# Kernel tuning notes

Measured on AMD Instinct MI355X. Metric: run time of the kernel, lower is better.

The kernel has to match this reference:

```python
import jax, jax.numpy as jnp
import numpy as np
from jax import lax

B, N, K = 8, 4096, 16          # clouds, points per cloud, knn neighbors
RATIO = 0.5
M = int(N * RATIO)             # sampled points per cloud (fps ratio)
C_IN, C_OUT = 64, 128
EPS = 1e-5                      # BatchNorm eps


def setup_inputs() -> dict:
    key = jax.random.key(0)
    ks = jax.random.split(key, 4)
    x = jax.random.normal(ks[0], (B * N, C_IN), jnp.float32)
    pos = jax.random.uniform(ks[1], (B * N, 3), jnp.float32)
    batch = jnp.repeat(jnp.arange(B, dtype=jnp.int32), N)
    W = jax.random.normal(ks[2], (C_IN, C_OUT), jnp.float32) / np.sqrt(C_IN).astype(np.float32)
    b = jnp.zeros((C_OUT,), jnp.float32)
    gamma = jnp.ones((C_OUT,), jnp.float32)
    beta = jnp.zeros((C_OUT,), jnp.float32)
    return {"x": x, "pos": pos, "batch": batch, "W": W, "b": b, "gamma": gamma, "beta": beta}


def _fps(pos_c):
    # Farthest point sampling on one cloud. pos_c: [N,3] -> [M] local indices.
    # Deterministic start at index 0 (reference for torch_cluster.fps).
    def step(carry, _):
        dmin, last = carry
        d = jnp.sum((pos_c - pos_c[last]) ** 2, axis=-1)   # [N]
        dmin = jnp.minimum(dmin, d)
        nxt = jnp.argmax(dmin).astype(jnp.int32)
        return (dmin, nxt), last
    init = (jnp.full((pos_c.shape[0],), jnp.inf, pos_c.dtype), jnp.int32(0))
    _, idx = lax.scan(step, init, None, length=M)
    return idx


def _knn(pos_c, qpos_c):
    # k nearest original points for each sampled point. [N,3],[M,3] -> [M,K].
    d = jnp.sum((qpos_c[:, None, :] - pos_c[None, :, :]) ** 2, axis=-1)  # [M,N]
    _, idx = lax.top_k(-d, K)
    return idx


def reference(x, pos, batch, W, b, gamma, beta):
    pos_b = pos.reshape(B, N, 3)
    fps_idx = jax.vmap(_fps)(pos_b)                                       # [B,M]
    new_pos_b = jnp.take_along_axis(pos_b, fps_idx[:, :, None], axis=1)   # [B,M,3]
    nbr = jax.vmap(_knn)(pos_b, new_pos_b)                                # [B,M,K]

    # mlp: Linear -> BatchNorm1d (training-mode batch stats) -> GELU
    h = x @ W + b                                                         # [B*N,C_OUT]
    mu = jnp.mean(h, axis=0)
    var = jnp.mean((h - mu) ** 2, axis=0)
    h = (h - mu) * lax.rsqrt(var + EPS) * gamma + beta
    h = jax.nn.gelu(h, approximate=False)
    h_b = h.reshape(B, N, C_OUT)

    # gather neighbor features; scatter-max over edge_index[0] == max over K
    # (each sampled point has exactly K incoming edges)
    feats = jax.vmap(lambda hb, nb: hb[nb])(h_b, nbr)                     # [B,M,K,C_OUT]
    new_x = jnp.max(feats, axis=2).reshape(B * M, C_OUT)
    new_pos = new_pos_b.reshape(B * M, 3)
    new_batch = jnp.repeat(jnp.arange(B, dtype=batch.dtype), M)
    return (new_x, new_pos, new_batch)
```

## Files before the change

### kernel.cpp

```cpp
#include <hip/hip_runtime.h>
#include <math.h>

#define NB 8
#define NN 4096
#define MM 2048
#define KNN_K 16
#define CIN 64
#define COUT 128
#define BN_EPS 1e-5f

typedef float v2f __attribute__((ext_vector_type(2)));

__device__ __forceinline__ v2f pk_add(v2f a, v2f b) {
  v2f r;
  asm("v_pk_add_f32 %0, %1, %2" : "=v"(r) : "v"(a), "v"(b));
  return r;
}
__device__ __forceinline__ v2f pk_mul(v2f a, v2f b) {
  v2f r;
  asm("v_pk_mul_f32 %0, %1, %2" : "=v"(r) : "v"(a), "v"(b));
  return r;
}

__device__ __forceinline__ double pack_key(float d, unsigned code) {
  return __longlong_as_double(
      (long long)(((unsigned long long)__float_as_uint(d) << 32) | code));
}
__device__ __forceinline__ unsigned unpack_code(double v) {
  return (unsigned)((unsigned long long)__double_as_longlong(v) &
                    0xFFFFFFFFull);
}

__device__ __forceinline__ float sqdist_np(float dx, float dy, float dz) {
  return __fadd_rn(__fadd_rn(__fmul_rn(dx, dx), __fmul_rn(dy, dy)),
                   __fmul_rn(dz, dz));
}

#define DPP_MAX_LEVEL(best, ctrl, rmask)                                     \
  {                                                                          \
    const int _lo = __builtin_amdgcn_update_dpp(                             \
        __double2loint(best), __double2loint(best), (ctrl), (rmask), 0xf,    \
        false);                                                              \
    const int _hi = __builtin_amdgcn_update_dpp(                             \
        __double2hiint(best), __double2hiint(best), (ctrl), (rmask), 0xf,    \
        false);                                                              \
    best = fmax(best, __hiloint2double(_hi, _lo));                           \
  }
#define DPP_MIN_LEVEL(best, ctrl, rmask)                                     \
  {                                                                          \
    const int _lo = __builtin_amdgcn_update_dpp(                             \
        __double2loint(best), __double2loint(best), (ctrl), (rmask), 0xf,    \
        false);                                                              \
    const int _hi = __builtin_amdgcn_update_dpp(                             \
        __double2hiint(best), __double2hiint(best), (ctrl), (rmask), 0xf,    \
        false);                                                              \
    best = fmin(best, __hiloint2double(_hi, _lo));                           \
  }

__global__ __launch_bounds__(256) void k_fps_gemm(
    const float* __restrict__ pos, const float* __restrict__ x,
    const float* __restrict__ W, const float* __restrict__ bias,
    float* __restrict__ h, float* __restrict__ gsum,
    float* __restrict__ gsumsq, int* __restrict__ fps_idx,
    float* __restrict__ out_pos, float* __restrict__ out_batch) {
  __shared__ __align__(16) char smem_raw[57472];
  const int tid = threadIdx.x;

  if (blockIdx.x < NB) {
    float* xs = (float*)smem_raw;
    float* ys = xs + NN;
    float* zs = ys + NN;
    int* idxs = (int*)(smem_raw + 49152);
    double* red = (double*)(smem_raw + 57344);
    const int b = blockIdx.x;
    const float* posc = pos + (size_t)b * NN * 3;
    for (int i = tid; i < NN; i += 256) {
      xs[i] = posc[i * 3 + 0];
      ys[i] = posc[i * 3 + 1];
      zs[i] = posc[i * 3 + 2];
    }
    __syncthreads();

    v2f pxv[8], pyv[8], pzv[8];
    double key[16];
    const unsigned code_base = (unsigned)(NN - 1 - tid * 16);
#pragma unroll
    for (int u = 0; u < 8; ++u) {
      const int p = tid * 16 + 2 * u;
      pxv[u] = (v2f){xs[p], xs[p + 1]};
      pyv[u] = (v2f){ys[p], ys[p + 1]};
      pzv[u] = (v2f){zs[p], zs[p + 1]};
    }
#pragma unroll
    for (int s = 0; s < 16; ++s)
      key[s] = __hiloint2double(0x7f800000, (int)(code_base - s));

    const int lane = tid & 63, wv = tid >> 6;
    int last = 0;
    if (tid == 0) idxs[0] = 0;
    float lx = xs[0], ly = ys[0], lz = zs[0];
    for (int m = 1; m < MM; ++m) {
      const v2f nlx = {-lx, -lx}, nly = {-ly, -ly}, nlz = {-lz, -lz};
      double b0 = 0.0, b1 = 0.0, b2 = 0.0, b3 = 0.0;
#pragma unroll
      for (int u = 0; u < 8; ++u) {
        const v2f dx = pk_add(pxv[u], nlx);
        const v2f dy = pk_add(pyv[u], nly);
        const v2f dz = pk_add(pzv[u], nlz);
        const v2f d2 =
            pk_add(pk_add(pk_mul(dx, dx), pk_mul(dy, dy)), pk_mul(dz, dz));
        const int s0 = 2 * u, s1 = 2 * u + 1;
        const float n0 =
            fminf(__int_as_float(__double2hiint(key[s0])), d2.x);
        const float n1 =
            fminf(__int_as_float(__double2hiint(key[s1])), d2.y);
        key[s0] = __hiloint2double(__float_as_int(n0), (int)(code_base - s0));
        key[s1] = __hiloint2double(__float_as_int(n1), (int)(code_base - s1));
        switch (u & 3) {
          case 0: b0 = fmax(b0, fmax(key[s0], key[s1])); break;
          case 1: b1 = fmax(b1, fmax(key[s0], key[s1])); break;
          case 2: b2 = fmax(b2, fmax(key[s0], key[s1])); break;
          default: b3 = fmax(b3, fmax(key[s0], key[s1])); break;
        }
      }
      double best = fmax(fmax(b0, b1), fmax(b2, b3));
      DPP_MAX_LEVEL(best, 0x121, 0xf);
      DPP_MAX_LEVEL(best, 0x122, 0xf);
      DPP_MAX_LEVEL(best, 0x124, 0xf);
      DPP_MAX_LEVEL(best, 0x128, 0xf);
      DPP_MAX_LEVEL(best, 0x142, 0xa);
      DPP_MAX_LEVEL(best, 0x143, 0xc);
      const int par = (m & 1) * 4;
      if (lane == 63) red[par + wv] = best;
      __syncthreads();
      const double f = fmax(fmax(red[par + 0], red[par + 1]),
                            fmax(red[par + 2], red[par + 3]));
      last = (NN - 1) - (int)unpack_code(f);
      if (tid == 0) idxs[m] = last;
      lx = xs[last];
      ly = ys[last];
      lz = zs[last];
    }
    __syncthreads();
    for (int m = tid; m < MM; m += 256) {
      const int p = idxs[m];
      const int o = b * MM + m;
      fps_idx[o] = p;
      out_pos[o * 3 + 0] = xs[p];
      out_pos[o * 3 + 1] = ys[p];
      out_pos[o * 3 + 2] = zs[p];
      out_batch[o] = (float)b;
    }
  } else {
    float* Wl = (float*)smem_raw;
    float* xl = Wl + CIN * COUT;
    float* bsum = (float*)(smem_raw + 49152);
    float* bsq = bsum + COUT;
    const int bid = blockIdx.x - NB;
    const int r0 = bid * 64;
    for (int i = tid; i < CIN * COUT; i += 256) Wl[i] = W[i];
    for (int i = tid; i < 64 * CIN; i += 256) xl[i] = x[(size_t)r0 * CIN + i];
    if (tid < 2 * COUT) bsum[tid] = 0.f;
    __syncthreads();
    const int cg = tid & 31, rg = tid >> 5;
    const int c = cg * 4;
    float acc[8][4];
#pragma unroll
    for (int j = 0; j < 8; ++j)
#pragma unroll
      for (int t = 0; t < 4; ++t) acc[j][t] = 0.f;
    for (int k = 0; k < CIN; ++k) {
      const float4 wk = *(const float4*)&Wl[k * COUT + c];
#pragma unroll
      for (int j = 0; j < 8; ++j) {
        const float xv = xl[(rg * 8 + j) * CIN + k];
        acc[j][0] = fmaf(xv, wk.x, acc[j][0]);
        acc[j][1] = fmaf(xv, wk.y, acc[j][1]);
        acc[j][2] = fmaf(xv, wk.z, acc[j][2]);
        acc[j][3] = fmaf(xv, wk.w, acc[j][3]);
      }
    }
    const float4 bb = *(const float4*)&bias[c];
    float s0 = 0, s1 = 0, s2 = 0, s3 = 0, q0 = 0, q1 = 0, q2 = 0, q3 = 0;
#pragma unroll
    for (int j = 0; j < 8; ++j) {
      float4 hv;
      hv.x = acc[j][0] + bb.x;
      hv.y = acc[j][1] + bb.y;
      hv.z = acc[j][2] + bb.z;
      hv.w = acc[j][3] + bb.w;
      *(float4*)&h[(size_t)(r0 + rg * 8 + j) * COUT + c] = hv;
      s0 += hv.x; s1 += hv.y; s2 += hv.z; s3 += hv.w;
      q0 += hv.x * hv.x; q1 += hv.y * hv.y;
      q2 += hv.z * hv.z; q3 += hv.w * hv.w;
    }
    atomicAdd(&bsum[c + 0], s0); atomicAdd(&bsum[c + 1], s1);
    atomicAdd(&bsum[c + 2], s2); atomicAdd(&bsum[c + 3], s3);
    atomicAdd(&bsq[c + 0], q0);  atomicAdd(&bsq[c + 1], q1);
    atomicAdd(&bsq[c + 2], q2);  atomicAdd(&bsq[c + 3], q3);
    __syncthreads();
    if (tid < COUT) {
      atomicAdd(&gsum[tid], bsum[tid]);
      atomicAdd(&gsumsq[tid], bsq[tid]);
    }
  }
}

__device__ __forceinline__ float gelu_exact(float v) {
  return 0.5f * v * (1.0f + erff(v * 0.70710678118654752f));
}

__global__ __launch_bounds__(256) void k_knn(
    const float* __restrict__ pos, const int* __restrict__ fps_idx,
    const float* __restrict__ h, const float* __restrict__ gsum,
    const float* __restrict__ gsumsq, const float* __restrict__ gamma,
    const float* __restrict__ beta, float* __restrict__ out_x) {
  __shared__ float dc[4][NN];
  __shared__ float sc[COUT], sh[COUT];
  const int tid = threadIdx.x, lane = tid & 63, wv = tid >> 6;
  if (tid < COUT) {
    const float n = (float)(NB * NN);
    const float mu = gsum[tid] / n;
    const float var = gsumsq[tid] / n - mu * mu;
    const float rs = rsqrtf(var + BN_EPS);
    const float s = rs * gamma[tid];
    sc[tid] = s;
    sh[tid] = beta[tid] - mu * s;
  }
  __syncthreads();
  const int b = blockIdx.x & 7;
  const int m = (blockIdx.x >> 3) * 4 + wv;
  const int q = b * MM + m;
  const int qi = fps_idx[q];
  const float* posc = pos + (size_t)b * NN * 3;
  const float qx = posc[qi * 3 + 0], qy = posc[qi * 3 + 1],
              qz = posc[qi * 3 + 2];
  float* dcw = dc[wv];
  const double DINF = __longlong_as_double(0x7FF0000000000000LL);
  double gmin[8];
#pragma unroll
  for (int g = 0; g < 8; ++g) gmin[g] = DINF;
#pragma unroll
  for (int s = 0; s < 64; ++s) {
    const int p = s * 64 + lane;
    const float d = sqdist_np(posc[p * 3 + 0] - qx, posc[p * 3 + 1] - qy,
                              posc[p * 3 + 2] - qz);
    dcw[p] = d;
    gmin[s >> 3] = fmin(gmin[s >> 3], pack_key(d, (unsigned)p));
  }
  double lmin = gmin[0];
#pragma unroll
  for (int g = 1; g < 8; ++g) lmin = fmin(lmin, gmin[g]);

  int nbr[KNN_K];
#pragma unroll
  for (int r = 0; r < KNN_K; ++r) {
    double v = lmin;
    DPP_MIN_LEVEL(v, 0x121, 0xf);
    DPP_MIN_LEVEL(v, 0x122, 0xf);
    DPP_MIN_LEVEL(v, 0x124, 0xf);
    DPP_MIN_LEVEL(v, 0x128, 0xf);
    DPP_MIN_LEVEL(v, 0x142, 0xa);
    DPP_MIN_LEVEL(v, 0x143, 0xc);
    const unsigned p =
        (unsigned)__builtin_amdgcn_readlane(__double2loint(v), 63);
    nbr[r] = (int)p;
    if (lane == (int)(p & 63)) {
      dcw[p] = __int_as_float(0x7f800000);
      const int g = (int)(p >> 9);
      double nm = DINF;
      const int base = g * 8 * 64 + lane;
#pragma unroll
      for (int j = 0; j < 8; ++j) {
        const int pp = base + j * 64;
        nm = fmin(nm, pack_key(dcw[pp], (unsigned)pp));
      }
#pragma unroll
      for (int gg = 0; gg < 8; ++gg)
        if (gg == g) gmin[gg] = nm;
      lmin = gmin[0];
#pragma unroll
      for (int gg = 1; gg < 8; ++gg) lmin = fmin(lmin, gmin[gg]);
    }
  }

  const float* hb = h + (size_t)b * NN * COUT;
  const float PINF = __int_as_float(0x7f800000);
  float mx0 = -PINF, mn0 = PINF, mx1 = -PINF, mn1 = PINF;
#pragma unroll
  for (int r = 0; r < KNN_K; ++r) {
    const float* row = hb + (size_t)nbr[r] * COUT;
    const float a = row[lane], c = row[lane + 64];
    mx0 = fmaxf(mx0, a);
    mn0 = fminf(mn0, a);
    mx1 = fmaxf(mx1, c);
    mn1 = fminf(mn1, c);
  }
  const float sc0 = sc[lane], sh0 = sh[lane];
  const float sc1 = sc[lane + 64], sh1 = sh[lane + 64];
  const float o0 = fmaxf(gelu_exact(fmaf(mx0, sc0, sh0)),
                         gelu_exact(fmaf(mn0, sc0, sh0)));
  const float o1 = fmaxf(gelu_exact(fmaf(mx1, sc1, sh1)),
                         gelu_exact(fmaf(mn1, sc1, sh1)));
  out_x[(size_t)q * COUT + lane] = o0;
  out_x[(size_t)q * COUT + lane + 64] = o1;
}

extern "C" void kernel_launch(void* const* d_in, const int* in_sizes, int n_in,
                              void* d_out, int out_size, void* d_ws,
                              size_t ws_size, hipStream_t stream) {
  const float* x = (const float*)d_in[0];
  const float* pos = (const float*)d_in[1];
  const float* W = (const float*)d_in[3];
  const float* bias = (const float*)d_in[4];
  const float* gamma = (const float*)d_in[5];
  const float* beta = (const float*)d_in[6];

  float* out_x = (float*)d_out;
  float* out_pos = out_x + (size_t)NB * MM * COUT;
  float* out_batch = out_pos + (size_t)NB * MM * 3;

  char* ws = (char*)d_ws;
  float* h = (float*)ws;
  float* gsum = (float*)(ws + (size_t)16777216);
  float* gsumsq = gsum + COUT;
  int* fps_idx = (int*)(gsumsq + COUT);

  (void)hipMemsetAsync(gsum, 0, 2 * COUT * sizeof(float), stream);
  hipLaunchKernelGGL(k_fps_gemm, dim3(NB + 512), dim3(256), 0, stream, pos, x,
                     W, bias, h, gsum, gsumsq, fps_idx, out_pos, out_batch);
  hipLaunchKernelGGL(k_knn, dim3(4096), dim3(256), 0, stream, pos, fps_idx, h,
                     gsum, gsumsq, gamma, beta, out_x);
}
```

Measured before the change: 1.236 ms.

## Fuse FPS, GEMM and kNN into one persistent kernel streaming FPS indices

Merges the two kernels into one persistent launch. The 8 FPS blocks publish each sampled index to a global flag array as soon as it is chosen. 504 worker blocks first compute the GEMM tiles with BN statistics, wait on a global counter, then run kNN and the gather-max on published queries while FPS is still running. The kNN step now recomputes distances instead of caching them in LDS, which frees shared memory for higher occupancy. The design depends on all blocks being co-resident (spin-waits) and adds polling traffic and global atomics.

```diff
diff --git a/kernel.cpp b/kernel.cpp
--- a/kernel.cpp
+++ b/kernel.cpp
@@ -8,6 +8,8 @@
 #define CIN 64
 #define COUT 128
 #define BN_EPS 1e-5f
+#define NWORK 504
+#define NTILES 512
 
 typedef float v2f __attribute__((ext_vector_type(2)));
 
@@ -57,21 +59,27 @@
     best = fmin(best, __hiloint2double(_hi, _lo));                           \
   }
 
-__global__ __launch_bounds__(256) void k_fps_gemm(
+__device__ __forceinline__ float gelu_exact(float v) {
+  return 0.5f * v * (1.0f + erff(v * 0.70710678118654752f));
+}
+
+__global__ __launch_bounds__(256, 3) void k_fused(
     const float* __restrict__ pos, const float* __restrict__ x,
     const float* __restrict__ W, const float* __restrict__ bias,
+    const float* __restrict__ gamma, const float* __restrict__ beta,
     float* __restrict__ h, float* __restrict__ gsum,
-    float* __restrict__ gsumsq, int* __restrict__ fps_idx,
+    float* __restrict__ gsumsq, int* __restrict__ pub,
+    int* __restrict__ gemm_done, float* __restrict__ out_x,
     float* __restrict__ out_pos, float* __restrict__ out_batch) {
-  __shared__ __align__(16) char smem_raw[57472];
+  __shared__ __align__(16) char smem_raw[50176];
   const int tid = threadIdx.x;
+  const int lane = tid & 63, wv = tid >> 6;
 
   if (blockIdx.x < NB) {
     float* xs = (float*)smem_raw;
     float* ys = xs + NN;
     float* zs = ys + NN;
-    int* idxs = (int*)(smem_raw + 49152);
-    double* red = (double*)(smem_raw + 57344);
+    double* red = (double*)(smem_raw + 49152);
     const int b = blockIdx.x;
     const float* posc = pos + (size_t)b * NN * 3;
     for (int i = tid; i < NN; i += 256) {
@@ -95,10 +103,15 @@
     for (int s = 0; s < 16; ++s)
       key[s] = __hiloint2double(0x7f800000, (int)(code_base - s));
 
-    const int lane = tid & 63, wv = tid >> 6;
     int last = 0;
-    if (tid == 0) idxs[0] = 0;
     float lx = xs[0], ly = ys[0], lz = zs[0];
+    if (tid == 0) {
+      __hip_atomic_store(&pub[b * MM], 1, __ATOMIC_RELAXED,
+                         __HIP_MEMORY_SCOPE_AGENT);
+      out_pos[(size_t)(b * MM) * 3 + 0] = lx;
+      out_pos[(size_t)(b * MM) * 3 + 1] = ly;
+      out_pos[(size_t)(b * MM) * 3 + 2] = lz;
+    }
     for (int m = 1; m < MM; ++m) {
       const v2f nlx = {-lx, -lx}, nly = {-ly, -ly}, nlz = {-lz, -lz};
       double b0 = 0.0, b1 = 0.0, b2 = 0.0, b3 = 0.0;
@@ -136,174 +149,201 @@
       const double f = fmax(fmax(red[par + 0], red[par + 1]),
                             fmax(red[par + 2], red[par + 3]));
       last = (NN - 1) - (int)unpack_code(f);
-      if (tid == 0) idxs[m] = last;
       lx = xs[last];
       ly = ys[last];
       lz = zs[last];
-    }
-    __syncthreads();
-    for (int m = tid; m < MM; m += 256) {
-      const int p = idxs[m];
-      const int o = b * MM + m;
-      fps_idx[o] = p;
-      out_pos[o * 3 + 0] = xs[p];
-      out_pos[o * 3 + 1] = ys[p];
-      out_pos[o * 3 + 2] = zs[p];
-      out_batch[o] = (float)b;
-    }
+      if (tid == 0) {
+        const int o = b * MM + m;
+        __hip_atomic_store(&pub[o], last + 1, __ATOMIC_RELAXED,
+                           __HIP_MEMORY_SCOPE_AGENT);
+        out_pos[(size_t)o * 3 + 0] = lx;
+        out_pos[(size_t)o * 3 + 1] = ly;
+        out_pos[(size_t)o * 3 + 2] = lz;
+      }
+    }
+    for (int m = tid; m < MM; m += 256) out_batch[b * MM + m] = (float)b;
   } else {
+    const int wkr = blockIdx.x - NB;
     float* Wl = (float*)smem_raw;
     float* xl = Wl + CIN * COUT;
     float* bsum = (float*)(smem_raw + 49152);
     float* bsq = bsum + COUT;
-    const int bid = blockIdx.x - NB;
-    const int r0 = bid * 64;
-    for (int i = tid; i < CIN * COUT; i += 256) Wl[i] = W[i];
-    for (int i = tid; i < 64 * CIN; i += 256) xl[i] = x[(size_t)r0 * CIN + i];
-    if (tid < 2 * COUT) bsum[tid] = 0.f;
+#pragma unroll 1
+    for (int rep = 0; rep < 2; ++rep) {
+      if (rep == 1 && wkr >= NTILES - NWORK) break;
+      const int t = rep ? (NWORK + wkr) : wkr;
+      const int r0 = t * 64;
+      for (int i = tid; i < CIN * COUT; i += 256) Wl[i] = W[i];
+      for (int i = tid; i < 64 * CIN; i += 256)
+        xl[i] = x[(size_t)r0 * CIN + i];
+      bsum[tid] = 0.f;
+      __syncthreads();
+      const int cg = tid & 31, rg = tid >> 5;
+      const int c = cg * 4;
+      float acc[8][4];
+#pragma unroll
+      for (int j = 0; j < 8; ++j)
+#pragma unroll
+        for (int tt = 0; tt < 4; ++tt) acc[j][tt] = 0.f;
+      for (int k = 0; k < CIN; ++k) {
+        const float4 wk = *(const float4*)&Wl[k * COUT + c];
+#pragma unroll
+        for (int j = 0; j < 8; ++j) {
+          const float xv = xl[(rg * 8 + j) * CIN + k];
+          acc[j][0] = fmaf(xv, wk.x, acc[j][0]);
+          acc[j][1] = fmaf(xv, wk.y, acc[j][1]);
+          acc[j][2] = fmaf(xv, wk.z, acc[j][2]);
+          acc[j][3] = fmaf(xv, wk.w, acc[j][3]);
+        }
+      }
+      const float4 bb = *(const float4*)&bias[c];
+      float s0 = 0, s1 = 0, s2 = 0, s3 = 0, q0 = 0, q1 = 0, q2 = 0, q3 = 0;
+#pragma unroll
+      for (int j = 0; j < 8; ++j) {
+        float4 hv;
+        hv.x = acc[j][0] + bb.x;
+        hv.y = acc[j][1] + bb.y;
+        hv.z = acc[j][2] + bb.z;
+        hv.w = acc[j][3] + bb.w;
+        *(float4*)&h[(size_t)(r0 + rg * 8 + j) * COUT + c] = hv;
+        s0 += hv.x; s1 += hv.y; s2 += hv.z; s3 += hv.w;
+        q0 += hv.x * hv.x; q1 += hv.y * hv.y;
+        q2 += hv.z * hv.z; q3 += hv.w * hv.w;
+      }
+      atomicAdd(&bsum[c + 0], s0); atomicAdd(&bsum[c + 1], s1);
+      atomicAdd(&bsum[c + 2], s2); atomicAdd(&bsum[c + 3], s3);
+      atomicAdd(&bsq[c + 0], q0);  atomicAdd(&bsq[c + 1], q1);
+      atomicAdd(&bsq[c + 2], q2);  atomicAdd(&bsq[c + 3], q3);
+      __syncthreads();
+      if (tid < COUT) {
+        atomicAdd(&gsum[tid], bsum[tid]);
+        atomicAdd(&gsumsq[tid], bsq[tid]);
+      }
+      __syncthreads();
+      if (tid == 0) {
+        __threadfence();
+        atomicAdd(gemm_done, 1);
+      }
+    }
+
+    if (tid == 0) {
+      while (__hip_atomic_load(gemm_done, __ATOMIC_RELAXED,
+                               __HIP_MEMORY_SCOPE_AGENT) < NTILES)
+        __builtin_amdgcn_s_sleep(64);
+    }
     __syncthreads();
-    const int cg = tid & 31, rg = tid >> 5;
-    const int c = cg * 4;
-    float acc[8][4];
-#pragma unroll
-    for (int j = 0; j < 8; ++j)
-#pragma unroll
-      for (int t = 0; t < 4; ++t) acc[j][t] = 0.f;
-    for (int k = 0; k < CIN; ++k) {
-      const float4 wk = *(const float4*)&Wl[k * COUT + c];
-#pragma unroll
-      for (int j = 0; j < 8; ++j) {
-        const float xv = xl[(rg * 8 + j) * CIN + k];
-        acc[j][0] = fmaf(xv, wk.x, acc[j][0]);
-        acc[j][1] = fmaf(xv, wk.y, acc[j][1]);
-        acc[j][2] = fmaf(xv, wk.z, acc[j][2]);
-        acc[j][3] = fmaf(xv, wk.w, acc[j][3]);
-      }
-    }
-    const float4 bb = *(const float4*)&bias[c];
-    float s0 = 0, s1 = 0, s2 = 0, s3 = 0, q0 = 0, q1 = 0, q2 = 0, q3 = 0;
-#pragma unroll
-    for (int j = 0; j < 8; ++j) {
-      float4 hv;
-      hv.x = acc[j][0] + bb.x;
-      hv.y = acc[j][1] + bb.y;
-      hv.z = acc[j][2] + bb.z;
-      hv.w = acc[j][3] + bb.w;
-      *(float4*)&h[(size_t)(r0 + rg * 8 + j) * COUT + c] = hv;
-      s0 += hv.x; s1 += hv.y; s2 += hv.z; s3 += hv.w;
-      q0 += hv.x * hv.x; q1 += hv.y * hv.y;
-      q2 += hv.z * hv.z; q3 += hv.w * hv.w;
-    }
-    atomicAdd(&bsum[c + 0], s0); atomicAdd(&bsum[c + 1], s1);
-    atomicAdd(&bsum[c + 2], s2); atomicAdd(&bsum[c + 3], s3);
-    atomicAdd(&bsq[c + 0], q0);  atomicAdd(&bsq[c + 1], q1);
-    atomicAdd(&bsq[c + 2], q2);  atomicAdd(&bsq[c + 3], q3);
+    __threadfence();
+
+    float* scs = (float*)smem_raw;
+    float* shs = scs + COUT;
+    if (tid < COUT) {
+      const float n = (float)(NB * NN);
+      const float su = __hip_atomic_load(&gsum[tid], __ATOMIC_RELAXED,
+                                         __HIP_MEMORY_SCOPE_AGENT);
+      const float sq = __hip_atomic_load(&gsumsq[tid], __ATOMIC_RELAXED,
+                                         __HIP_MEMORY_SCOPE_AGENT);
+      const float mu = su / n;
+      const float var = sq / n - mu * mu;
+      const float rs = rsqrtf(var + BN_EPS);
+      const float s = rs * gamma[tid];
+      scs[tid] = s;
+      shs[tid] = beta[tid] - mu * s;
+    }
     __syncthreads();
-    if (tid < COUT) {
-      atomicAdd(&gsum[tid], bsum[tid]);
-      atomicAdd(&gsumsq[tid], bsq[tid]);
+
+    const int b = wkr & 7;
+    const int widx = (wkr >> 3) * 4 + wv;
+    const float sc0 = scs[lane], sh0 = shs[lane];
+    const float sc1 = scs[lane + 64], sh1 = shs[lane + 64];
+    const double DINF = __longlong_as_double(0x7FF0000000000000LL);
+    const float PINF = __int_as_float(0x7f800000);
+    const float* posc = pos + (size_t)b * NN * 3;
+    const float* hb = h + (size_t)b * NN * COUT;
+    const int* pubc = pub + b * MM;
+
+    for (int m = widx; m < MM; m += 252) {
+      int pv = __hip_atomic_load(&pubc[m], __ATOMIC_RELAXED,
+                                 __HIP_MEMORY_SCOPE_AGENT);
+      while (pv == 0) {
+        __builtin_amdgcn_s_sleep(2);
+        pv = __hip_atomic_load(&pubc[m], __ATOMIC_RELAXED,
+                               __HIP_MEMORY_SCOPE_AGENT);
+      }
+      const int qi = pv - 1;
+      const float qx = posc[qi * 3 + 0], qy = posc[qi * 3 + 1],
+                  qz = posc[qi * 3 + 2];
+      double gmin[8];
+#pragma unroll
+      for (int g = 0; g < 8; ++g) gmin[g] = DINF;
+      unsigned long long rm = 0ull;
+#pragma unroll
+      for (int s = 0; s < 64; ++s) {
+        const int p = (s << 6) + lane;
+        const float d = sqdist_np(posc[p * 3 + 0] - qx, posc[p * 3 + 1] - qy,
+                                  posc[p * 3 + 2] - qz);
+        gmin[s >> 3] = fmin(gmin[s >> 3], pack_key(d, (unsigned)p));
+      }
+      double lmin = gmin[0];
+#pragma unroll
+      for (int g = 1; g < 8; ++g) lmin = fmin(lmin, gmin[g]);
+
+      int nbr[KNN_K];
+#pragma unroll
+      for (int r = 0; r < KNN_K; ++r) {
+        double v = lmin;
+        DPP_MIN_LEVEL(v, 0x121, 0xf);
+        DPP_MIN_LEVEL(v, 0x122, 0xf);
+        DPP_MIN_LEVEL(v, 0x124, 0xf);
+        DPP_MIN_LEVEL(v, 0x128, 0xf);
+        DPP_MIN_LEVEL(v, 0x142, 0xa);
+        DPP_MIN_LEVEL(v, 0x143, 0xc);
+        const unsigned p =
+            (unsigned)__builtin_amdgcn_readlane(__double2loint(v), 63);
+        nbr[r] = (int)p;
+        if (lane == (int)(p & 63)) {
+          const int sr = (int)(p >> 6);
+          rm |= (1ull << sr);
+          const int g = sr >> 3;
+          double nm = DINF;
+#pragma unroll
+          for (int j = 0; j < 8; ++j) {
+            const int s2 = (g << 3) + j;
+            const int pp = (s2 << 6) + lane;
+            const float d =
+                sqdist_np(posc[pp * 3 + 0] - qx, posc[pp * 3 + 1] - qy,
+                          posc[pp * 3 + 2] - qz);
+            double kk = pack_key(d, (unsigned)pp);
+            if ((rm >> s2) & 1ull) kk = DINF;
+            nm = fmin(nm, kk);
+          }
+#pragma unroll
+          for (int gg = 0; gg < 8; ++gg)
+            if (gg == g) gmin[gg] = nm;
+          lmin = gmin[0];
+#pragma unroll
+          for (int gg = 1; gg < 8; ++gg) lmin = fmin(lmin, gmin[gg]);
+        }
+      }
+
+      float mx0 = -PINF, mn0 = PINF, mx1 = -PINF, mn1 = PINF;
+#pragma unroll
+      for (int r = 0; r < KNN_K; ++r) {
+        const float* row = hb + (size_t)nbr[r] * COUT;
+        const float a = row[lane], cc = row[lane + 64];
+        mx0 = fmaxf(mx0, a);
+        mn0 = fminf(mn0, a);
+        mx1 = fmaxf(mx1, cc);
+        mn1 = fminf(mn1, cc);
+      }
+      const int q = b * MM + m;
+      const float o0 = fmaxf(gelu_exact(fmaf(mx0, sc0, sh0)),
+                             gelu_exact(fmaf(mn0, sc0, sh0)));
+      const float o1 = fmaxf(gelu_exact(fmaf(mx1, sc1, sh1)),
+                             gelu_exact(fmaf(mn1, sc1, sh1)));
+      out_x[(size_t)q * COUT + lane] = o0;
+      out_x[(size_t)q * COUT + lane + 64] = o1;
     }
   }
-}
-
-__device__ __forceinline__ float gelu_exact(float v) {
-  return 0.5f * v * (1.0f + erff(v * 0.70710678118654752f));
-}
-
-__global__ __launch_bounds__(256) void k_knn(
-    const float* __restrict__ pos, const int* __restrict__ fps_idx,
-    const float* __restrict__ h, const float* __restrict__ gsum,
-    const float* __restrict__ gsumsq, const float* __restrict__ gamma,
-    const float* __restrict__ beta, float* __restrict__ out_x) {
-  __shared__ float dc[4][NN];
-  __shared__ float sc[COUT], sh[COUT];
-  const int tid = threadIdx.x, lane = tid & 63, wv = tid >> 6;
-  if (tid < COUT) {
-    const float n = (float)(NB * NN);
-    const float mu = gsum[tid] / n;
-    const float var = gsumsq[tid] / n - mu * mu;
-    const float rs = rsqrtf(var + BN_EPS);
-    const float s = rs * gamma[tid];
-    sc[tid] = s;
-    sh[tid] = beta[tid] - mu * s;
-  }
-  __syncthreads();
-  const int b = blockIdx.x & 7;
-  const int m = (blockIdx.x >> 3) * 4 + wv;
-  const int q = b * MM + m;
-  const int qi = fps_idx[q];
-  const float* posc = pos + (size_t)b * NN * 3;
-  const float qx = posc[qi * 3 + 0], qy = posc[qi * 3 + 1],
-              qz = posc[qi * 3 + 2];
-  float* dcw = dc[wv];
-  const double DINF = __longlong_as_double(0x7FF0000000000000LL);
-  double gmin[8];
-#pragma unroll
-  for (int g = 0; g < 8; ++g) gmin[g] = DINF;
-#pragma unroll
-  for (int s = 0; s < 64; ++s) {
-    const int p = s * 64 + lane;
-    const float d = sqdist_np(posc[p * 3 + 0] - qx, posc[p * 3 + 1] - qy,
-                              posc[p * 3 + 2] - qz);
-    dcw[p] = d;
-    gmin[s >> 3] = fmin(gmin[s >> 3], pack_key(d, (unsigned)p));
-  }
-  double lmin = gmin[0];
-#pragma unroll
-  for (int g = 1; g < 8; ++g) lmin = fmin(lmin, gmin[g]);
-
-  int nbr[KNN_K];
-#pragma unroll
-  for (int r = 0; r < KNN_K; ++r) {
-    double v = lmin;
-    DPP_MIN_LEVEL(v, 0x121, 0xf);
-    DPP_MIN_LEVEL(v, 0x122, 0xf);
-    DPP_MIN_LEVEL(v, 0x124, 0xf);
-    DPP_MIN_LEVEL(v, 0x128, 0xf);
-    DPP_MIN_LEVEL(v, 0x142, 0xa);
-    DPP_MIN_LEVEL(v, 0x143, 0xc);
-    const unsigned p =
-        (unsigned)__builtin_amdgcn_readlane(__double2loint(v), 63);
-    nbr[r] = (int)p;
-    if (lane == (int)(p & 63)) {
-      dcw[p] = __int_as_float(0x7f800000);
-      const int g = (int)(p >> 9);
-      double nm = DINF;
-      const int base = g * 8 * 64 + lane;
-#pragma unroll
-      for (int j = 0; j < 8; ++j) {
-        const int pp = base + j * 64;
-        nm = fmin(nm, pack_key(dcw[pp], (unsigned)pp));
-      }
-#pragma unroll
-      for (int gg = 0; gg < 8; ++gg)
-        if (gg == g) gmin[gg] = nm;
-      lmin = gmin[0];
-#pragma unroll
-      for (int gg = 1; gg < 8; ++gg) lmin = fmin(lmin, gmin[gg]);
-    }
-  }
-
-  const float* hb = h + (size_t)b * NN * COUT;
-  const float PINF = __int_as_float(0x7f800000);
-  float mx0 = -PINF, mn0 = PINF, mx1 = -PINF, mn1 = PINF;
-#pragma unroll
-  for (int r = 0; r < KNN_K; ++r) {
-    const float* row = hb + (size_t)nbr[r] * COUT;
-    const float a = row[lane], c = row[lane + 64];
-    mx0 = fmaxf(mx0, a);
-    mn0 = fminf(mn0, a);
-    mx1 = fmaxf(mx1, c);
-    mn1 = fminf(mn1, c);
-  }
-  const float sc0 = sc[lane], sh0 = sh[lane];
-  const float sc1 = sc[lane + 64], sh1 = sh[lane + 64];
-  const float o0 = fmaxf(gelu_exact(fmaf(mx0, sc0, sh0)),
-                         gelu_exact(fmaf(mn0, sc0, sh0)));
-  const float o1 = fmaxf(gelu_exact(fmaf(mx1, sc1, sh1)),
-                         gelu_exact(fmaf(mn1, sc1, sh1)));
-  out_x[(size_t)q * COUT + lane] = o0;
-  out_x[(size_t)q * COUT + lane + 64] = o1;
 }
 
 extern "C" void kernel_launch(void* const* d_in, const int* in_sizes, int n_in,
@@ -324,11 +364,13 @@
   float* h = (float*)ws;
   float* gsum = (float*)(ws + (size_t)16777216);
   float* gsumsq = gsum + COUT;
-  int* fps_idx = (int*)(gsumsq + COUT);
-
-  (void)hipMemsetAsync(gsum, 0, 2 * COUT * sizeof(float), stream);
-  hipLaunchKernelGGL(k_fps_gemm, dim3(NB + 512), dim3(256), 0, stream, pos, x,
-                     W, bias, h, gsum, gsumsq, fps_idx, out_pos, out_batch);
-  hipLaunchKernelGGL(k_knn, dim3(4096), dim3(256), 0, stream, pos, fps_idx, h,
-                     gsum, gsumsq, gamma, beta, out_x);
-}
+  int* pub = (int*)(gsumsq + COUT);
+  int* gemm_done = pub + NB * MM;
+
+  (void)hipMemsetAsync(gsum, 0, 2 * COUT * sizeof(float) +
+                                     NB * MM * sizeof(int) + sizeof(int),
+                       stream);
+  hipLaunchKernelGGL(k_fused, dim3(NB + NWORK), dim3(256), 0, stream, pos, x,
+                     W, bias, gamma, beta, h, gsum, gsumsq, pub, gemm_done,
+                     out_x, out_pos, out_batch);
+}
```

Result: no change. 1.233 ms (-0.2%).
